# Kernel optimization log

Hardware: AMD Instinct MI355X
Metric: run time of the kernel (lower is better)

Reference implementation:

```python
import jax, jax.numpy as jnp
import numpy as np
import math

THETA = 10000.0

def apply_rope(x, start_pos=0):
    # x: [B, H, S, D], rotate-half RoPE
    B, H, S, D = x.shape
    pos = jnp.arange(start_pos, start_pos + S, dtype=jnp.float32)
    inv_freq = 1.0 / (THETA ** (jnp.arange(0, D, 2, dtype=jnp.float32) / D))  # [D/2]
    ang = pos[:, None] * inv_freq[None, :]  # [S, D/2]
    cos, sin = jnp.cos(ang), jnp.sin(ang)
    x1, x2 = jnp.split(x, 2, axis=-1)
    return jnp.concatenate([x1 * cos - x2 * sin, x1 * sin + x2 * cos], axis=-1)


def setup_inputs() -> dict:
    key = jax.random.key(0)
    ks = jax.random.split(key, 9)
    B, S, E, H, D = 2, 2048, 2048, 16, 128
    s = 0.02
    return {
        "x": jax.random.normal(ks[0], (B, S, E), jnp.float32),
        "W_q": jax.random.normal(ks[1], (E, H * D), jnp.float32) * s,
        "b_q": jnp.zeros((H * D,), jnp.float32),
        "W_k": jax.random.normal(ks[2], (E, D), jnp.float32) * s,
        "b_k": jnp.zeros((D,), jnp.float32),
        "W_v": jax.random.normal(ks[3], (E, D), jnp.float32) * s,
        "b_v": jnp.zeros((D,), jnp.float32),
        "W_o": jax.random.normal(ks[4], (H * D, E), jnp.float32) * s,
        "b_o": jnp.zeros((E,), jnp.float32),
    }


def reference(x, W_q, b_q, W_k, b_k, W_v, b_v, W_o, b_o):
    B, S, E = x.shape
    D = W_k.shape[1]
    H = W_q.shape[1] // D
    # projections (weights stored [in, out])
    q = (x @ W_q + b_q).reshape(B, S, H, D).transpose(0, 2, 1, 3)   # [B,H,S,D]
    k = (x @ W_k + b_k).reshape(B, S, 1, D).transpose(0, 2, 1, 3)   # [B,1,S,D]
    v = (x @ W_v + b_v).reshape(B, S, 1, D).transpose(0, 2, 1, 3)   # [B,1,S,D]
    # RoPE (cache is None -> start_pos = 0)
    q = apply_rope(q, 0)
    k = apply_rope(k, 0)
    # shared-KV attention: k head dim broadcasts over H q heads
    scores = jnp.einsum("bhqd,bokd->bhqk", q, k) / math.sqrt(D)     # [B,H,S,S]
    causal = jnp.tril(jnp.ones((S, S), dtype=bool))
    scores = jnp.where(causal, scores, -jnp.inf)
    attn = jax.nn.softmax(scores, axis=-1)
    out = jnp.einsum("bhqk,bokd->bhqd", attn, v)                    # [B,H,S,D]
    out = out.transpose(0, 2, 1, 3).reshape(B, S, H * D)
    out = out @ W_o + b_o                                           # dropout is identity in eval
    return out
```

## Files before the change

### kernel.cpp

```cpp
#include <hip/hip_runtime.h>
#include <stdint.h>

typedef __bf16 bf16x8 __attribute__((ext_vector_type(8)));
typedef __bf16 bf16x2 __attribute__((ext_vector_type(2)));
typedef float  f32x4  __attribute__((ext_vector_type(4)));
typedef short  s16x8  __attribute__((ext_vector_type(8)));

__device__ inline unsigned short f2b(float f) {
  unsigned int u = __builtin_bit_cast(unsigned int, f);
  u += 0x7FFFu + ((u >> 16) & 1u);
  return (unsigned short)(u >> 16);
}
__device__ inline float b2f(unsigned short h) {
  unsigned int u = ((unsigned int)h) << 16;
  return __builtin_bit_cast(float, u);
}
__device__ inline unsigned int pkcvt(float a, float b) {
  bf16x2 t;
  t[0] = (__bf16)a;
  t[1] = (__bf16)b;
  return __builtin_bit_cast(unsigned int, t);
}
__device__ inline void gload_lds16(const void* g, void* l) {
  __builtin_amdgcn_global_load_lds(
      (const __attribute__((address_space(1))) unsigned int*)g,
      (__attribute__((address_space(3))) unsigned int*)l, 16, 0, 0);
}

__global__ void k_cvt_bf16(const float* __restrict__ in, unsigned short* __restrict__ out, int n4) {
  int i = blockIdx.x * blockDim.x + threadIdx.x;
  if (i < n4) {
    float4 v = ((const float4*)in)[i];
    ushort4 o;
    o.x = f2b(v.x); o.y = f2b(v.y); o.z = f2b(v.z); o.w = f2b(v.w);
    ((ushort4*)out)[i] = o;
  }
}

__global__ void k_transpose(const float* __restrict__ A, int nA,
                            const float* __restrict__ Bsrc, int nB,
                            const float* __restrict__ Csrc,
                            unsigned short* __restrict__ dst, int K) {
  __shared__ float tile[32][33];
  int n0 = blockIdx.x * 32;
  int k0 = blockIdx.y * 32;
  const float* src; int ldn, noff;
  if (n0 < nA)            { src = A;    ldn = nA; noff = n0; }
  else if (n0 < nA + nB)  { src = Bsrc; ldn = nB; noff = n0 - nA; }
  else                    { src = Csrc; ldn = nB; noff = n0 - nA - nB; }
  int tx = threadIdx.x & 31, ty = threadIdx.x >> 5;
  for (int yy = ty; yy < 32; yy += 8)
    tile[yy][tx] = src[(size_t)(k0 + yy) * ldn + noff + tx];
  __syncthreads();
  for (int yy = ty; yy < 32; yy += 8)
    dst[(size_t)(n0 + yy) * K + k0 + tx] = f2b(tile[tx][yy]);
}

__global__ void k_bias_concat(const float* __restrict__ bq, const float* __restrict__ bk,
                              const float* __restrict__ bv, float* __restrict__ dst) {
  int i = blockIdx.x * 256 + threadIdx.x;
  if (i < 2304) dst[i] = (i < 2048) ? bq[i] : (i < 2176 ? bk[i - 2048] : bv[i - 2176]);
}

template<int OUT_BF16>
__global__ __launch_bounds__(256)
void k_gemm_lds(const unsigned short* __restrict__ A, const unsigned short* __restrict__ Bt,
                const float* __restrict__ bias, void* __restrict__ Cout,
                int M, int N, int K) {
  __shared__ unsigned short As[2][4096];
  __shared__ unsigned short Bs[2][4096];
  const int tid  = threadIdx.x;
  const int lane = tid & 63, wid = tid >> 6;
  const int lr = lane & 15, lk = lane >> 4;
  const int wr = wid >> 1,  wc = wid & 1;
  const int mb = blockIdx.y * 128, nb = blockIdx.x * 128;

  const int srow = tid >> 2, scb = (tid & 3) * 8;
  const size_t gA = (size_t)(mb + srow) * K + scb;
  const size_t gB = (size_t)(nb + srow) * K + scb;
  const int ldso = wid * 512;

  f32x4 acc[4][4];
  #pragma unroll
  for (int i = 0; i < 4; ++i)
    #pragma unroll
    for (int j = 0; j < 4; ++j) acc[i][j] = (f32x4){0.f, 0.f, 0.f, 0.f};

  auto stage = [&](int buf, int kt) {
    const size_t ko = (size_t)kt * 32;
    gload_lds16(A  + gA + ko,            &As[buf][ldso]);
    gload_lds16(A  + gA + 64 * (size_t)K + ko, &As[buf][2048 + ldso]);
    gload_lds16(Bt + gB + ko,            &Bs[buf][ldso]);
    gload_lds16(Bt + gB + 64 * (size_t)K + ko, &Bs[buf][2048 + ldso]);
  };

  const int ktn = K >> 5;
  stage(0, 0);
  __syncthreads();

  int cur = 0;
  #pragma unroll 1
  for (int kt = 0; kt < ktn; ++kt) {
    if (kt + 1 < ktn) stage(cur ^ 1, kt + 1);
    bf16x8 af[4], bfv[4];
    #pragma unroll
    for (int m = 0; m < 4; ++m)
      af[m]  = *(const bf16x8*)&As[cur][(wr * 64 + m * 16 + lr) * 32 + lk * 8];
    #pragma unroll
    for (int n = 0; n < 4; ++n)
      bfv[n] = *(const bf16x8*)&Bs[cur][(wc * 64 + n * 16 + lr) * 32 + lk * 8];
    #pragma unroll
    for (int m = 0; m < 4; ++m)
      #pragma unroll
      for (int n = 0; n < 4; ++n)
        acc[m][n] = __builtin_amdgcn_mfma_f32_16x16x32_bf16(af[m], bfv[n], acc[m][n], 0, 0, 0);
    __syncthreads();
    cur ^= 1;
  }

  const int r0 = mb + wr * 64, c0 = nb + wc * 64;
  #pragma unroll
  for (int m = 0; m < 4; ++m) {
    #pragma unroll
    for (int n = 0; n < 4; ++n) {
      int col = c0 + n * 16 + lr;
      float bb = bias[col];
      #pragma unroll
      for (int r = 0; r < 4; ++r) {
        int row = r0 + m * 16 + lk * 4 + r;
        float v = acc[m][n][r] + bb;
        if (OUT_BF16) ((unsigned short*)Cout)[(size_t)row * N + col] = f2b(v);
        else          ((float*)Cout)[(size_t)row * N + col] = v;
      }
    }
  }
}

__global__ void k_rope(const unsigned short* __restrict__ qkv,
                       unsigned short* __restrict__ qr,
                       unsigned short* __restrict__ kr,
                       int S, int H) {
  int R = blockIdx.x * 4 + (threadIdx.x >> 6);
  int lane = threadIdx.x & 63;
  int per_b = S * (H + 1);
  int b = R / per_b;
  int rem = R - b * per_b;
  int s = rem / (H + 1);
  int j = rem - s * (H + 1);
  const unsigned short* src = qkv + (size_t)(b * S + s) * 2304 + (j < H ? j * 128 : 2048);
  float x1 = b2f(src[lane]);
  float x2 = b2f(src[lane + 64]);
  float invf = expf(-(float)lane * (9.210340371976184f / 64.0f));
  float ang = (float)s * invf;
  float c = cosf(ang), sn = sinf(ang);
  float o1 = x1 * c - x2 * sn;
  float o2 = x1 * sn + x2 * c;
  unsigned short* dst;
  if (j < H) {
    const float scale = 0.08838834764831845f;
    o1 *= scale; o2 *= scale;
    dst = qr + ((size_t)(b * H + j) * S + s) * 128;
  } else {
    dst = kr + ((size_t)(b * S) + s) * 128;
  }
  dst[lane]      = f2b(o1);
  dst[lane + 64] = f2b(o2);
}

__global__ void k_vtrans(const unsigned short* __restrict__ qkv,
                         unsigned short* __restrict__ vt, int S) {
  __shared__ unsigned short tile[32][33];
  int b = blockIdx.z;
  int s0 = blockIdx.x * 32, d0 = blockIdx.y * 32;
  int tx = threadIdx.x & 31, ty = threadIdx.x >> 5;
  for (int yy = ty; yy < 32; yy += 8)
    tile[yy][tx] = qkv[(size_t)(b * S + s0 + yy) * 2304 + 2176 + d0 + tx];
  __syncthreads();
  for (int yy = ty; yy < 32; yy += 8)
    vt[((size_t)b * 128 + d0 + yy) * S + s0 + tx] = tile[tx][yy];
}

__global__ __launch_bounds__(256)
void k_attn(const unsigned short* __restrict__ qr,
            const unsigned short* __restrict__ kr,
            const unsigned short* __restrict__ vt,
            unsigned short* __restrict__ attn_out,
            int S, int H) {
  const int b = blockIdx.z, h = blockIdx.y;
  const int tid = threadIdx.x, wid = tid >> 6, lane = tid & 63;
  const int lr = lane & 15, lk = lane >> 4;

  __shared__ unsigned short Kt[2][64 * 128];
  __shared__ unsigned short Vt[2][128 * 64];
  __shared__ unsigned short P_all[4][16][72];
  unsigned short (*P)[72] = P_all[wid];

  const char* kbyte = (const char*)(kr + (size_t)b * S * 128);
  const char* vbyte = (const char*)(vt + (size_t)b * 128 * S);
  const size_t vrow_bytes = (size_t)S * 2;

  const int krow0 = tid >> 4;
  const int kcb   = (tid & 15) << 4;
  const int vd0   = tid >> 3;
  const int vcb   = (tid & 7) << 4;
  const int lds_woff = (wid * 1024) >> 1;

  const int ksw = (lr & 7) << 4;

  const int ntiles = gridDim.x * 2;

  #pragma unroll 1
  for (int half = 0; half < 2; ++half) {
    const int qt  = (half == 0) ? blockIdx.x : (ntiles - 1 - blockIdx.x);
    const int qb0 = qt * 64;
    const int qw  = qb0 + wid * 16;

    const unsigned short* qptr = qr + ((size_t)(b * H + h) * S + (qw + lr)) * 128;
    bf16x8 aq[4];
    #pragma unroll
    for (int kk = 0; kk < 4; ++kk) aq[kk] = *(const bf16x8*)(qptr + kk * 32 + lk * 8);

    f32x4 accO[8];
    #pragma unroll
    for (int t = 0; t < 8; ++t) accO[t] = (f32x4){0.f, 0.f, 0.f, 0.f};
    float lsum = 0.f;

    auto stage = [&](int buf, int kb) {
      const char* kg = kbyte + (size_t)kb * 256;
      #pragma unroll
      for (int r = 0; r < 4; ++r) {
        int row = krow0 + r * 16;
        const char* src = kg + row * 256 + (kcb ^ ((row & 7) << 4));
        gload_lds16(src, (void*)(&Kt[buf][0] + lds_woff + r * 2048));
      }
      const char* vg = vbyte + (size_t)kb * 2;
      #pragma unroll
      for (int r = 0; r < 4; ++r) {
        int d = vd0 + r * 32;
        const char* src = vg + (size_t)d * vrow_bytes + (vcb ^ ((d & 7) << 4));
        gload_lds16(src, (void*)(&Vt[buf][0] + lds_woff + r * 2048));
      }
    };

    int cur = 0;
    stage(0, 0);
    __syncthreads();

    #pragma unroll 1
    for (int kb = 0; kb <= qb0; kb += 64) {
      if (kb + 64 <= qb0) stage(cur ^ 1, kb + 64);
      const bool diag = (kb == qb0);
      const unsigned short* Kc = &Kt[cur][0];
      const unsigned short* Vc = &Vt[cur][0];

      bf16x8 kf[4][4];
      #pragma unroll
      for (int m = 0; m < 4; ++m) {
        const char* kl = (const char*)(Kc + (m * 16 + lr) * 128);
        #pragma unroll
        for (int kk = 0; kk < 4; ++kk)
          kf[m][kk] = *(const bf16x8*)(kl + ((kk * 64 + lk * 16) ^ ksw));
      }
      f32x4 s4[4];
      #pragma unroll
      for (int m = 0; m < 4; ++m) s4[m] = (f32x4){0.f, 0.f, 0.f, 0.f};
      __builtin_amdgcn_s_setprio(1);
      #pragma unroll
      for (int kk = 0; kk < 4; ++kk)
        #pragma unroll
        for (int m = 0; m < 4; ++m)
          s4[m] = __builtin_amdgcn_mfma_f32_16x16x32_bf16(kf[m][kk], aq[kk], s4[m], 0, 0, 0);
      __builtin_amdgcn_s_setprio(0);

      #pragma unroll
      for (int m = 0; m < 4; ++m) {
        float p[4];
        #pragma unroll
        for (int r = 0; r < 4; ++r) {
          float v = __expf(s4[m][r]);
          if (diag && (m * 16 + lk * 4 + r) > (wid * 16 + lr)) v = 0.f;
          p[r] = v;
          lsum += v;
        }
        uint2 w;
        w.x = pkcvt(p[0], p[1]);
        w.y = pkcvt(p[2], p[3]);
        *(uint2*)&P[lr][m * 16 + lk * 4] = w;
      }

      #pragma unroll
      for (int ks = 0; ks < 2; ++ks) {
        bf16x8 pa = *(const bf16x8*)&P[lr][ks * 32 + lk * 8];
        __builtin_amdgcn_s_setprio(1);
        #pragma unroll
        for (int t = 0; t < 8; ++t) {
          const char* vl = (const char*)(Vc + (t * 16 + lr) * 64);
          bf16x8 bv = *(const bf16x8*)(vl + ((ks * 64 + lk * 16) ^ ksw));
          accO[t] = __builtin_amdgcn_mfma_f32_16x16x32_bf16(pa, bv, accO[t], 0, 0, 0);
        }
        __builtin_amdgcn_s_setprio(0);
      }
      __syncthreads();
      cur ^= 1;
    }

    lsum += __shfl_xor(lsum, 16);
    lsum += __shfl_xor(lsum, 32);
    float rl[4];
    #pragma unroll
    for (int r = 0; r < 4; ++r) rl[r] = 1.0f / __shfl(lsum, lk * 4 + r);
    #pragma unroll
    for (int t = 0; t < 8; ++t) {
      #pragma unroll
      for (int r = 0; r < 4; ++r) {
        int srow = qw + lk * 4 + r;
        float o = accO[t][r] * rl[r];
        attn_out[((size_t)(b * S) + srow) * 2048 + h * 128 + t * 16 + lr] = f2b(o);
      }
    }
  }
}

extern "C" void kernel_launch(void* const* d_in, const int* in_sizes, int n_in,
                              void* d_out, int out_size, void* d_ws, size_t ws_size,
                              hipStream_t stream) {
  const float* x  = (const float*)d_in[0];
  const float* Wq = (const float*)d_in[1];
  const float* bq = (const float*)d_in[2];
  const float* Wk = (const float*)d_in[3];
  const float* bk = (const float*)d_in[4];
  const float* Wv = (const float*)d_in[5];
  const float* bv = (const float*)d_in[6];
  const float* Wo = (const float*)d_in[7];
  const float* bo = (const float*)d_in[8];

  const int B = 2, S = 2048, E = 2048, H = 16, D = 128;
  const int M = B * S;
  const int Nqkv = H * D + 2 * D;

  char* w = (char*)d_ws;
  unsigned short* xb    = (unsigned short*)w;
  unsigned short* WqkvT = (unsigned short*)(w + 16777216);
  unsigned short* qkv   = (unsigned short*)(w + 16777216 + 9437184);
  unsigned short* qr    = (unsigned short*)(w + 16777216 + 9437184 + 18874368);
  unsigned short* kr    = qr + (size_t)B * H * S * D;
  unsigned short* vtb   = kr + (size_t)B * S * D;
  float*          cbias = (float*)(vtb + (size_t)B * S * D);
  unsigned short* attn_out = xb;
  unsigned short* WoT      = WqkvT;

  k_cvt_bf16<<<dim3((M * E / 4) / 256), 256, 0, stream>>>(x, xb, M * E / 4);
  k_transpose<<<dim3(Nqkv / 32, E / 32), 256, 0, stream>>>(Wq, H * D, Wk, D, Wv, WqkvT, E);
  k_bias_concat<<<dim3(9), 256, 0, stream>>>(bq, bk, bv, cbias);
  k_gemm_lds<1><<<dim3(Nqkv / 128, M / 128), 256, 0, stream>>>(xb, WqkvT, cbias, (void*)qkv, M, Nqkv, E);
  k_rope<<<dim3(B * S * (H + 1) / 4), 256, 0, stream>>>(qkv, qr, kr, S, H);
  k_vtrans<<<dim3(S / 32, D / 32, B), 256, 0, stream>>>(qkv, vtb, S);
  k_transpose<<<dim3(E / 32, (H * D) / 32), 256, 0, stream>>>(Wo, E, nullptr, 0, nullptr, WoT, H * D);
  k_attn<<<dim3(S / 128, H, B), 256, 0, stream>>>(qr, kr, vtb, attn_out, S, H);
  k_gemm_lds<0><<<dim3(E / 128, M / 128), 256, 0, stream>>>(attn_out, WoT, bo, (void*)d_out, M, E, H * D);
}
```

Before: 213.2 us.

## Use partial vmcnt waits in GEMM/attention pipelines and merge weight transposes

In the GEMM and attention loops, the full __syncthreads drain after each prefetch is replaced by explicit s_waitcnt vmcnt(N) plus s_barrier. This waits only for the current buffer's async global-to-LDS loads, so the next tile's loads stay in flight during compute. The Wo transpose is also folded into the QKV weight transpose launch as a second z-slice, writing to a separate workspace region, which removes one kernel launch. The risks are correctness if the vmcnt counts don't match the number of outstanding loads, and extra workspace use for WoT.

Measured after the change: 208.6 us. 1.02x faster.

```diff
diff --git a/kernel.cpp b/kernel.cpp
--- a/kernel.cpp
+++ b/kernel.cpp
@@ -37,17 +37,24 @@
   }
 }
 
-__global__ void k_transpose(const float* __restrict__ A, int nA,
-                            const float* __restrict__ Bsrc, int nB,
-                            const float* __restrict__ Csrc,
-                            unsigned short* __restrict__ dst, int K) {
+__global__ void k_transpose(const float* __restrict__ Wq, const float* __restrict__ Wk,
+                            const float* __restrict__ Wv, const float* __restrict__ Wo,
+                            unsigned short* __restrict__ dstQKV, unsigned short* __restrict__ dstO) {
   __shared__ float tile[32][33];
   int n0 = blockIdx.x * 32;
   int k0 = blockIdx.y * 32;
-  const float* src; int ldn, noff;
-  if (n0 < nA)            { src = A;    ldn = nA; noff = n0; }
-  else if (n0 < nA + nB)  { src = Bsrc; ldn = nB; noff = n0 - nA; }
-  else                    { src = Csrc; ldn = nB; noff = n0 - nA - nB; }
+  const float* src; int ldn, noff, K;
+  unsigned short* dst;
+  if (blockIdx.z == 0) {
+    K = 2048; dst = dstQKV;
+    if (n0 < 2048)       { src = Wq; ldn = 2048; noff = n0; }
+    else if (n0 < 2176)  { src = Wk; ldn = 128;  noff = n0 - 2048; }
+    else                 { src = Wv; ldn = 128;  noff = n0 - 2176; }
+  } else {
+    if (n0 >= 2048) return;
+    K = 2048; dst = dstO;
+    src = Wo; ldn = 2048; noff = n0;
+  }
   int tx = threadIdx.x & 31, ty = threadIdx.x >> 5;
   for (int yy = ty; yy < 32; yy += 8)
     tile[yy][tx] = src[(size_t)(k0 + yy) * ldn + noff + tx];
@@ -88,20 +95,26 @@
 
   auto stage = [&](int buf, int kt) {
     const size_t ko = (size_t)kt * 32;
-    gload_lds16(A  + gA + ko,            &As[buf][ldso]);
+    gload_lds16(A  + gA + ko,                  &As[buf][ldso]);
     gload_lds16(A  + gA + 64 * (size_t)K + ko, &As[buf][2048 + ldso]);
-    gload_lds16(Bt + gB + ko,            &Bs[buf][ldso]);
+    gload_lds16(Bt + gB + ko,                  &Bs[buf][ldso]);
     gload_lds16(Bt + gB + 64 * (size_t)K + ko, &Bs[buf][2048 + ldso]);
   };
 
   const int ktn = K >> 5;
   stage(0, 0);
-  __syncthreads();
 
   int cur = 0;
   #pragma unroll 1
   for (int kt = 0; kt < ktn; ++kt) {
-    if (kt + 1 < ktn) stage(cur ^ 1, kt + 1);
+    if (kt + 1 < ktn) {
+      stage(cur ^ 1, kt + 1);
+      asm volatile("s_waitcnt vmcnt(4)" ::: "memory");
+    } else {
+      asm volatile("s_waitcnt vmcnt(0)" ::: "memory");
+    }
+    __builtin_amdgcn_sched_barrier(0);
+    __builtin_amdgcn_s_barrier();
     bf16x8 af[4], bfv[4];
     #pragma unroll
     for (int m = 0; m < 4; ++m)
@@ -114,7 +127,7 @@
       #pragma unroll
       for (int n = 0; n < 4; ++n)
         acc[m][n] = __builtin_amdgcn_mfma_f32_16x16x32_bf16(af[m], bfv[n], acc[m][n], 0, 0, 0);
-    __syncthreads();
+    __builtin_amdgcn_s_barrier();
     cur ^= 1;
   }
 
@@ -244,11 +257,17 @@
 
     int cur = 0;
     stage(0, 0);
-    __syncthreads();
 
     #pragma unroll 1
     for (int kb = 0; kb <= qb0; kb += 64) {
-      if (kb + 64 <= qb0) stage(cur ^ 1, kb + 64);
+      if (kb + 64 <= qb0) {
+        stage(cur ^ 1, kb + 64);
+        asm volatile("s_waitcnt vmcnt(8)" ::: "memory");
+      } else {
+        asm volatile("s_waitcnt vmcnt(0)" ::: "memory");
+      }
+      __builtin_amdgcn_sched_barrier(0);
+      __builtin_amdgcn_s_barrier();
       const bool diag = (kb == qb0);
       const unsigned short* Kc = &Kt[cur][0];
       const unsigned short* Vc = &Vt[cur][0];
@@ -300,7 +319,7 @@
         }
         __builtin_amdgcn_s_setprio(0);
       }
-      __syncthreads();
+      __builtin_amdgcn_s_barrier();
       cur ^= 1;
     }
 
@@ -346,16 +365,15 @@
   unsigned short* kr    = qr + (size_t)B * H * S * D;
   unsigned short* vtb   = kr + (size_t)B * S * D;
   float*          cbias = (float*)(vtb + (size_t)B * S * D);
+  unsigned short* WoT   = (unsigned short*)(cbias + 4096);
   unsigned short* attn_out = xb;
-  unsigned short* WoT      = WqkvT;
 
   k_cvt_bf16<<<dim3((M * E / 4) / 256), 256, 0, stream>>>(x, xb, M * E / 4);
-  k_transpose<<<dim3(Nqkv / 32, E / 32), 256, 0, stream>>>(Wq, H * D, Wk, D, Wv, WqkvT, E);
+  k_transpose<<<dim3(Nqkv / 32, E / 32, 2), 256, 0, stream>>>(Wq, Wk, Wv, Wo, WqkvT, WoT);
   k_bias_concat<<<dim3(9), 256, 0, stream>>>(bq, bk, bv, cbias);
   k_gemm_lds<1><<<dim3(Nqkv / 128, M / 128), 256, 0, stream>>>(xb, WqkvT, cbias, (void*)qkv, M, Nqkv, E);
   k_rope<<<dim3(B * S * (H + 1) / 4), 256, 0, stream>>>(qkv, qr, kr, S, H);
   k_vtrans<<<dim3(S / 32, D / 32, B), 256, 0, stream>>>(qkv, vtb, S);
-  k_transpose<<<dim3(E / 32, (H * D) / 32), 256, 0, stream>>>(Wo, E, nullptr, 0, nullptr, WoT, H * D);
   k_attn<<<dim3(S / 128, H, B), 256, 0, stream>>>(qr, kr, vtb, attn_out, S, H);
   k_gemm_lds<0><<<dim3(E / 128, M / 128), 256, 0, stream>>>(attn_out, WoT, bo, (void*)d_out, M, E, H * D);
 }
```
